# Performance work log

Hardware: AMD Instinct MI355X
Metric: run time of the kernel (lower is better)

## Reference

```python
import jax, jax.numpy as jnp
import numpy as np

B, S, D, H = 2, 2048, 1024, 16
HD = D // H
NEG_INF = jnp.finfo(jnp.float32).min


def setup_inputs() -> dict:
    key = jax.random.key(0)
    ks = jax.random.split(key, 6)
    s = 1.0 / np.sqrt(D)
    return {
        'x': jax.random.normal(ks[0], (B, S, D), dtype=jnp.float32),
        'Wq': jax.random.normal(ks[1], (D, D), dtype=jnp.float32) * s,
        'Wk': jax.random.normal(ks[2], (D, D), dtype=jnp.float32) * s,
        'Wv': jax.random.normal(ks[3], (D, D), dtype=jnp.float32) * s,
        'Wo': jax.random.normal(ks[4], (D, D), dtype=jnp.float32) * s,
        'bo': jnp.zeros((D,), dtype=jnp.float32),
    }


def reference(x, Wq, Wk, Wv, Wo, bo):
    b, s, _ = x.shape
    scale = HD ** -0.5
    # Q/K/V projections: einsum('bnd,di->bni') == x @ W
    def proj(W):
        return jnp.einsum('bnd,di->bni', x, W).reshape(b, s, H, HD).transpose(0, 2, 1, 3)
    Q, K, V = proj(Wq), proj(Wk), proj(Wv)  # [b,h,s,hd]
    scores = jnp.einsum('bhnd,bhmd->bhnm', Q, K) * scale  # [b,h,s,s]
    causal = jnp.tril(jnp.ones((s, s), dtype=bool))
    scores = jnp.where(causal[None, None], scores, NEG_INF)
    attn = jax.nn.softmax(scores, axis=-1)
    ctx = jnp.einsum('bhnm,bhmd->bhnd', attn, V)
    ctx = ctx.transpose(0, 2, 1, 3).reshape(b, s, D)
    # nn.Linear: ctx @ Wo.T + bo
    return jnp.einsum('bnd,od->bno', ctx, Wo) + bo
```

## Files before the change

### kernel.cpp

```cpp
#include <hip/hip_runtime.h>

#define B_  2
#define S_  2048
#define D_  1024
#define H_  16
#define HD_ 64
#define M_  (B_*S_)

typedef __attribute__((ext_vector_type(8))) short s16x8;
typedef __attribute__((ext_vector_type(4))) float f32x4;
typedef __attribute__((ext_vector_type(16))) float f32x16;

__device__ __forceinline__ unsigned short f2bf(float f) {
  unsigned int u = __builtin_bit_cast(unsigned int, f);
  u += 0x7fffu + ((u >> 16) & 1u);
  return (unsigned short)(u >> 16);
}

__device__ __forceinline__ void gload_lds16(const unsigned short* g, unsigned short* l) {
  __builtin_amdgcn_global_load_lds((const __attribute__((address_space(1))) void*)g,
                                   (__attribute__((address_space(3))) void*)l, 16, 0, 0);
}

__global__ void cvt_kernel(const float* __restrict__ in, unsigned short* __restrict__ out, int n4) {
  int i = blockIdx.x * blockDim.x + threadIdx.x;
  if (i >= n4) return;
  float4 v = reinterpret_cast<const float4*>(in)[i];
  ushort4 o;
  o.x = f2bf(v.x); o.y = f2bf(v.y); o.z = f2bf(v.z); o.w = f2bf(v.w);
  reinterpret_cast<ushort4*>(out)[i] = o;
}

__global__ void transpose_cvt3(const float* __restrict__ W0, const float* __restrict__ W1,
                               const float* __restrict__ W2, unsigned short* __restrict__ dstBase) {
  __shared__ float tile[32][33];
  const float* in = blockIdx.z == 0 ? W0 : (blockIdx.z == 1 ? W1 : W2);
  unsigned short* out = dstBase + (size_t)blockIdx.z * 1024 * 1024;
  const int bx = blockIdx.x, by = blockIdx.y, tx = threadIdx.x;
  const int x = bx * 32 + tx;
  for (int j = threadIdx.y; j < 32; j += 8)
    tile[j][tx] = in[(by * 32 + j) * 1024 + x];
  __syncthreads();
  const int xo = by * 32 + tx;
  for (int j = threadIdx.y; j < 32; j += 8)
    out[(bx * 32 + j) * 1024 + xo] = f2bf(tile[tx][j]);
}

#define BM 128
#define BN 128
#define BK 64

__global__ __launch_bounds__(256, 4) void gemm_bt(
    const unsigned short* __restrict__ A,
    const unsigned short* __restrict__ Bt,
    void* __restrict__ out0, void* __restrict__ out1, void* __restrict__ out2,
    const float* __restrict__ bias,
    const int mode, const float qscale)
{
  __shared__ unsigned short As[BM * BK];
  __shared__ unsigned short Bs[BN * BK];

  const int t    = threadIdx.x;
  const int lane = t & 63;
  const int wid  = t >> 6;
  const int l15  = lane & 15;
  const int g    = lane >> 4;
  const int wm   = wid >> 1;
  const int wn   = wid & 1;

  const int n0 = blockIdx.x * BN;
  const int m0 = blockIdx.y * BM;

  const int lrow = lane >> 3;
  const int lcol = ((lane & 7) ^ lrow) * 8;
  const int rsw  = l15 & 7;

  f32x4 acc[4][4];
#pragma unroll
  for (int i = 0; i < 4; ++i)
#pragma unroll
    for (int j = 0; j < 4; ++j)
      acc[i][j] = (f32x4){0.f, 0.f, 0.f, 0.f};

  for (int kt = 0; kt < 1024 / BK; ++kt) {
    const int k0 = kt * BK;
#pragma unroll
    for (int p = 0; p < 4; ++p) {
      const int c = p * 4 + wid;
      const int row = c * 8 + lrow;
      gload_lds16(&A[(size_t)(m0 + row) * 1024 + k0 + lcol], &As[c * 512]);
      gload_lds16(&Bt[(size_t)(n0 + row) * 1024 + k0 + lcol], &Bs[c * 512]);
    }
    __syncthreads();

#pragma unroll
    for (int kk = 0; kk < 2; ++kk) {
      s16x8 af[4], bf[4];
#pragma unroll
      for (int mi = 0; mi < 4; ++mi)
        af[mi] = *reinterpret_cast<const s16x8*>(
            &As[(wm * 64 + mi * 16 + l15) * BK + (((4 * kk + g) ^ rsw) * 8)]);
#pragma unroll
      for (int ni = 0; ni < 4; ++ni)
        bf[ni] = *reinterpret_cast<const s16x8*>(
            &Bs[(wn * 64 + ni * 16 + l15) * BK + (((4 * kk + g) ^ rsw) * 8)]);
#pragma unroll
      for (int mi = 0; mi < 4; ++mi)
#pragma unroll
        for (int ni = 0; ni < 4; ++ni)
          acc[mi][ni] = __builtin_amdgcn_mfma_f32_16x16x32_bf16(af[mi], bf[ni], acc[mi][ni], 0, 0, 0);
    }
    __syncthreads();
  }

  if (mode == 0) {
    const int sel = n0 >> 10;
    const int nl0 = n0 & 1023;
    if (sel < 2) {
      unsigned short* outb = (unsigned short*)(sel == 0 ? out0 : out1);
      const float sc = (sel == 0) ? qscale : 1.0f;
#pragma unroll
      for (int mi = 0; mi < 4; ++mi) {
#pragma unroll
        for (int ni = 0; ni < 4; ++ni) {
          const int n = nl0 + wn * 64 + ni * 16 + l15;
          const int h = n >> 6, hd = n & 63;
#pragma unroll
          for (int r = 0; r < 4; ++r) {
            const int m = m0 + wm * 64 + mi * 16 + 4 * g + r;
            const int b = m >> 11, s = m & 2047;
            outb[(((b * H_ + h) * S_) + s) * HD_ + hd] = f2bf(acc[mi][ni][r] * sc);
          }
        }
      }
    } else {
      unsigned short* outb = (unsigned short*)out2;
#pragma unroll
      for (int mi = 0; mi < 4; ++mi) {
#pragma unroll
        for (int ni = 0; ni < 4; ++ni) {
          const int n = nl0 + wn * 64 + ni * 16 + l15;
          const int h = n >> 6, hd = n & 63;
          const int m = m0 + wm * 64 + mi * 16 + 4 * g;
          const int b = m >> 11, s = m & 2047;
          ushort4 o;
          o.x = f2bf(acc[mi][ni][0]);
          o.y = f2bf(acc[mi][ni][1]);
          o.z = f2bf(acc[mi][ni][2]);
          o.w = f2bf(acc[mi][ni][3]);
          *reinterpret_cast<ushort4*>(&outb[(((b * H_ + h) * HD_) + hd) * S_ + s]) = o;
        }
      }
    }
  } else {
    float* outf = (float*)out0;
#pragma unroll
    for (int mi = 0; mi < 4; ++mi) {
#pragma unroll
      for (int ni = 0; ni < 4; ++ni) {
        const int n = n0 + wn * 64 + ni * 16 + l15;
        const float bv = bias[n];
#pragma unroll
        for (int r = 0; r < 4; ++r) {
          const int m = m0 + wm * 64 + mi * 16 + 4 * g + r;
          outf[m * 1024 + n] = acc[mi][ni][r] + bv;
        }
      }
    }
  }
}

__global__ __launch_bounds__(256) void attn_kernel(
    const unsigned short* __restrict__ Q,
    const unsigned short* __restrict__ K,
    const unsigned short* __restrict__ VT,
    unsigned short* __restrict__ Ctx)
{
  __shared__ unsigned short Kl[2][64 * 64];
  __shared__ unsigned short Vl[2][64 * 64];
  __shared__ unsigned short Pl[4][2][32][40];

  const int t    = threadIdx.x;
  const int lane = t & 63;
  const int w    = t >> 6;
  const int q    = lane & 31;
  const int hi   = lane >> 5;

  const int bh = blockIdx.x;
  const int qb = 15 - blockIdx.y;
  const long base  = (long)bh * S_ * HD_;
  const long vbase = (long)bh * HD_ * S_;
  const int q0w = qb * 128 + w * 32;

  const int srow = lane >> 3;
  const int scol = ((lane & 7) ^ srow) * 8;
  const int swz  = (q & 7) * 8;

  s16x8 qf[4];
#pragma unroll
  for (int s = 0; s < 4; ++s)
    qf[s] = *reinterpret_cast<const s16x8*>(&Q[base + (long)(q0w + q) * HD_ + 16 * s + 8 * hi]);

  f32x16 ctx0, ctx1;
#pragma unroll
  for (int r = 0; r < 16; ++r) { ctx0[r] = 0.f; ctx1[r] = 0.f; }
  float m_run = -1e30f, l_run = 0.f;

  const int nt = 2 * qb + 2;

#pragma unroll
  for (int p = 0; p < 2; ++p) {
    const int c = 2 * w + p;
    gload_lds16(&K[base + (long)(c * 8 + srow) * HD_ + scol], &Kl[0][c * 512]);
    gload_lds16(&VT[vbase + (long)(c * 8 + srow) * S_ + scol], &Vl[0][c * 512]);
  }
  __syncthreads();

  for (int kt = 0; kt < nt; ++kt) {
    const int cur  = kt & 1;
    const int kv64 = kt * 64;

    if (kt + 1 < nt) {
      const int nk = kv64 + 64;
#pragma unroll
      for (int p = 0; p < 2; ++p) {
        const int c = 2 * w + p;
        gload_lds16(&K[base + (long)(nk + c * 8 + srow) * HD_ + scol], &Kl[cur ^ 1][c * 512]);
        gload_lds16(&VT[vbase + (long)(c * 8 + srow) * S_ + nk + scol], &Vl[cur ^ 1][c * 512]);
      }
    }

    if (kv64 <= q0w + 31) {
      f32x16 sa0, sa1;
#pragma unroll
      for (int r = 0; r < 16; ++r) { sa0[r] = 0.f; sa1[r] = 0.f; }
      __builtin_amdgcn_s_setprio(1);
#pragma unroll
      for (int s = 0; s < 4; ++s) {
        const s16x8 kb0 = *reinterpret_cast<const s16x8*>(&Kl[cur][(q) * 64 + ((16 * s + 8 * hi) ^ swz)]);
        sa0 = __builtin_amdgcn_mfma_f32_32x32x16_bf16(kb0, qf[s], sa0, 0, 0, 0);
      }
#pragma unroll
      for (int s = 0; s < 4; ++s) {
        const s16x8 kb1 = *reinterpret_cast<const s16x8*>(&Kl[cur][(32 + q) * 64 + ((16 * s + 8 * hi) ^ swz)]);
        sa1 = __builtin_amdgcn_mfma_f32_32x32x16_bf16(kb1, qf[s], sa1, 0, 0, 0);
      }
      __builtin_amdgcn_s_setprio(0);

      if (kv64 + 64 > q0w) {
#pragma unroll
        for (int r = 0; r < 16; ++r) {
          const int kl = (r & 3) + 8 * (r >> 2) + 4 * hi;
          if (kv64 + kl > q0w + q)      sa0[r] = -1e30f;
          if (kv64 + 32 + kl > q0w + q) sa1[r] = -1e30f;
        }
      }

      float mx;
      {
        float a0 = fmaxf(fmaxf(sa0[0], sa0[1]), fmaxf(sa0[2], sa0[3]));
        float a1 = fmaxf(fmaxf(sa0[4], sa0[5]), fmaxf(sa0[6], sa0[7]));
        float a2 = fmaxf(fmaxf(sa0[8], sa0[9]), fmaxf(sa0[10], sa0[11]));
        float a3 = fmaxf(fmaxf(sa0[12], sa0[13]), fmaxf(sa0[14], sa0[15]));
        float b0 = fmaxf(fmaxf(sa1[0], sa1[1]), fmaxf(sa1[2], sa1[3]));
        float b1 = fmaxf(fmaxf(sa1[4], sa1[5]), fmaxf(sa1[6], sa1[7]));
        float b2 = fmaxf(fmaxf(sa1[8], sa1[9]), fmaxf(sa1[10], sa1[11]));
        float b3 = fmaxf(fmaxf(sa1[12], sa1[13]), fmaxf(sa1[14], sa1[15]));
        mx = fmaxf(fmaxf(fmaxf(a0, a1), fmaxf(a2, a3)), fmaxf(fmaxf(b0, b1), fmaxf(b2, b3)));
        mx = fmaxf(mx, __shfl_xor(mx, 32));
      }
      const float mn = fmaxf(m_run, mx);
      const float alpha = __builtin_amdgcn_exp2f(m_run - mn);
      m_run = mn;

      float p0[16], p1[16];
#pragma unroll
      for (int r = 0; r < 16; ++r) {
        p0[r] = __builtin_amdgcn_exp2f(sa0[r] - mn);
        p1[r] = __builtin_amdgcn_exp2f(sa1[r] - mn);
      }
      float ps;
      {
        float s0 = ((p0[0] + p0[1]) + (p0[2] + p0[3])) + ((p0[4] + p0[5]) + (p0[6] + p0[7]));
        float s1 = ((p0[8] + p0[9]) + (p0[10] + p0[11])) + ((p0[12] + p0[13]) + (p0[14] + p0[15]));
        float s2 = ((p1[0] + p1[1]) + (p1[2] + p1[3])) + ((p1[4] + p1[5]) + (p1[6] + p1[7]));
        float s3 = ((p1[8] + p1[9]) + (p1[10] + p1[11])) + ((p1[12] + p1[13]) + (p1[14] + p1[15]));
        ps = (s0 + s1) + (s2 + s3);
        ps += __shfl_xor(ps, 32);
      }
      l_run = l_run * alpha + ps;
#pragma unroll
      for (int r = 0; r < 16; ++r) { ctx0[r] *= alpha; ctx1[r] *= alpha; }

#pragma unroll
      for (int c = 0; c < 4; ++c) {
        unsigned int pk01, pk23;
        asm("v_cvt_pk_bf16_f32 %0, %1, %2" : "=v"(pk01) : "v"(p0[4 * c + 0]), "v"(p0[4 * c + 1]));
        asm("v_cvt_pk_bf16_f32 %0, %1, %2" : "=v"(pk23) : "v"(p0[4 * c + 2]), "v"(p0[4 * c + 3]));
        uint2 pr; pr.x = pk01; pr.y = pk23;
        *reinterpret_cast<uint2*>(&Pl[w][0][q][8 * c + 4 * hi]) = pr;
      }
#pragma unroll
      for (int c = 0; c < 4; ++c) {
        unsigned int pk01, pk23;
        asm("v_cvt_pk_bf16_f32 %0, %1, %2" : "=v"(pk01) : "v"(p1[4 * c + 0]), "v"(p1[4 * c + 1]));
        asm("v_cvt_pk_bf16_f32 %0, %1, %2" : "=v"(pk23) : "v"(p1[4 * c + 2]), "v"(p1[4 * c + 3]));
        uint2 pr; pr.x = pk01; pr.y = pk23;
        *reinterpret_cast<uint2*>(&Pl[w][1][q][8 * c + 4 * hi]) = pr;
      }

      __builtin_amdgcn_s_setprio(1);
#pragma unroll
      for (int kc = 0; kc < 4; ++kc) {
        const s16x8 pf = *reinterpret_cast<const s16x8*>(&Pl[w][kc >> 1][q][16 * (kc & 1) + 8 * hi]);
        const s16x8 v0 = *reinterpret_cast<const s16x8*>(&Vl[cur][(q) * 64 + ((16 * kc + 8 * hi) ^ swz)]);
        ctx0 = __builtin_amdgcn_mfma_f32_32x32x16_bf16(v0, pf, ctx0, 0, 0, 0);
        const s16x8 v1 = *reinterpret_cast<const s16x8*>(&Vl[cur][(32 + q) * 64 + ((16 * kc + 8 * hi) ^ swz)]);
        ctx1 = __builtin_amdgcn_mfma_f32_32x32x16_bf16(v1, pf, ctx1, 0, 0, 0);
      }
      __builtin_amdgcn_s_setprio(0);
    }

    __syncthreads();
  }

  const int b = bh >> 4, h = bh & 15;
  const float inv = 1.f / l_run;
  unsigned short* orow = &Ctx[((long)b * S_ + q0w + q) * D_ + h * 64];
#pragma unroll
  for (int c = 0; c < 4; ++c) {
    ushort4 o0, o1;
    o0.x = f2bf(ctx0[4 * c] * inv);     o0.y = f2bf(ctx0[4 * c + 1] * inv);
    o0.z = f2bf(ctx0[4 * c + 2] * inv); o0.w = f2bf(ctx0[4 * c + 3] * inv);
    o1.x = f2bf(ctx1[4 * c] * inv);     o1.y = f2bf(ctx1[4 * c + 1] * inv);
    o1.z = f2bf(ctx1[4 * c + 2] * inv); o1.w = f2bf(ctx1[4 * c + 3] * inv);
    *reinterpret_cast<ushort4*>(&orow[8 * c + 4 * hi])      = o0;
    *reinterpret_cast<ushort4*>(&orow[32 + 8 * c + 4 * hi]) = o1;
  }
}

extern "C" void kernel_launch(void* const* d_in, const int* in_sizes, int n_in,
                              void* d_out, int out_size, void* d_ws, size_t ws_size,
                              hipStream_t stream) {
  const float* x  = (const float*)d_in[0];
  const float* Wq = (const float*)d_in[1];
  const float* Wk = (const float*)d_in[2];
  const float* Wv = (const float*)d_in[3];
  const float* Wo = (const float*)d_in[4];
  const float* bo = (const float*)d_in[5];
  float* out = (float*)d_out;

  char* ws = (char*)d_ws;
  const size_t MB = 1024 * 1024;
  unsigned short* xb  = (unsigned short*)(ws + 0 * MB);
  unsigned short* WT  = (unsigned short*)(ws + 8 * MB);
  unsigned short* Wob = (unsigned short*)(ws + 14 * MB);
  unsigned short* Qb  = (unsigned short*)(ws + 16 * MB);
  unsigned short* Kb  = (unsigned short*)(ws + 24 * MB);
  unsigned short* VTb = (unsigned short*)(ws + 32 * MB);
  unsigned short* Cx  = (unsigned short*)(ws + 40 * MB);

  cvt_kernel<<<(M_ * D_ / 4 + 255) / 256, 256, 0, stream>>>(x, xb, M_ * D_ / 4);
  cvt_kernel<<<(D_ * D_ / 4 + 255) / 256, 256, 0, stream>>>(Wo, Wob, D_ * D_ / 4);
  transpose_cvt3<<<dim3(32, 32, 3), dim3(32, 8), 0, stream>>>(Wq, Wk, Wv, WT);

  gemm_bt<<<dim3(3 * D_ / BN, M_ / BM), 256, 0, stream>>>(
      xb, WT, (void*)Qb, (void*)Kb, (void*)VTb, nullptr, 0, 0.18033688011112042f);

  attn_kernel<<<dim3(B_ * H_, S_ / 128), 256, 0, stream>>>(Qb, Kb, VTb, Cx);

  gemm_bt<<<dim3(D_ / BN, M_ / BM), 256, 0, stream>>>(
      Cx, Wob, (void*)out, nullptr, nullptr, bo, 1, 1.0f);
}
```

Baseline: 124.2 us.

## Give each attention wave two query sub-tiles to reuse K/V fragments

The attention block drops from four waves to two. Each wave now handles 64 query rows as two 32-row sub-tiles, so K and V fragments are read from LDS once per tile and reused for both sub-tiles. The online softmax also adds a lazy rescale that only updates the running max and rescales the accumulators when the new max exceeds the old one by more than 8. This cuts LDS traffic and rescale work, but doubles register pressure per wave and halves the wave count per block, which can lower occupancy and latency hiding.

```diff
diff --git a/kernel.cpp b/kernel.cpp
--- a/kernel.cpp
+++ b/kernel.cpp
@@ -170,7 +170,7 @@
   }
 }
 
-__global__ __launch_bounds__(256) void attn_kernel(
+__global__ __launch_bounds__(128) void attn_kernel(
     const unsigned short* __restrict__ Q,
     const unsigned short* __restrict__ K,
     const unsigned short* __restrict__ VT,
@@ -178,7 +178,7 @@
 {
   __shared__ unsigned short Kl[2][64 * 64];
   __shared__ unsigned short Vl[2][64 * 64];
-  __shared__ unsigned short Pl[4][2][32][40];
+  __shared__ unsigned short Pl[2][2][32][40];
 
   const int t    = threadIdx.x;
   const int lane = t & 63;
@@ -190,27 +190,32 @@
   const int qb = 15 - blockIdx.y;
   const long base  = (long)bh * S_ * HD_;
   const long vbase = (long)bh * HD_ * S_;
-  const int q0w = qb * 128 + w * 32;
+  const int q0w = qb * 128 + w * 64;
 
   const int srow = lane >> 3;
   const int scol = ((lane & 7) ^ srow) * 8;
   const int swz  = (q & 7) * 8;
 
-  s16x8 qf[4];
-#pragma unroll
-  for (int s = 0; s < 4; ++s)
-    qf[s] = *reinterpret_cast<const s16x8*>(&Q[base + (long)(q0w + q) * HD_ + 16 * s + 8 * hi]);
-
-  f32x16 ctx0, ctx1;
-#pragma unroll
-  for (int r = 0; r < 16; ++r) { ctx0[r] = 0.f; ctx1[r] = 0.f; }
-  float m_run = -1e30f, l_run = 0.f;
+  s16x8 qf[2][4];
+#pragma unroll
+  for (int sub = 0; sub < 2; ++sub)
+#pragma unroll
+    for (int s = 0; s < 4; ++s)
+      qf[sub][s] = *reinterpret_cast<const s16x8*>(
+          &Q[base + (long)(q0w + 32 * sub + q) * HD_ + 16 * s + 8 * hi]);
+
+  f32x16 c0[2], c1[2];
+#pragma unroll
+  for (int sub = 0; sub < 2; ++sub)
+#pragma unroll
+    for (int r = 0; r < 16; ++r) { c0[sub][r] = 0.f; c1[sub][r] = 0.f; }
+  float ml[2] = {-1e30f, -1e30f}, ll[2] = {0.f, 0.f};
 
   const int nt = 2 * qb + 2;
 
 #pragma unroll
-  for (int p = 0; p < 2; ++p) {
-    const int c = 2 * w + p;
+  for (int p = 0; p < 4; ++p) {
+    const int c = 4 * w + p;
     gload_lds16(&K[base + (long)(c * 8 + srow) * HD_ + scol], &Kl[0][c * 512]);
     gload_lds16(&VT[vbase + (long)(c * 8 + srow) * S_ + scol], &Vl[0][c * 512]);
   }
@@ -223,119 +228,135 @@
     if (kt + 1 < nt) {
       const int nk = kv64 + 64;
 #pragma unroll
-      for (int p = 0; p < 2; ++p) {
-        const int c = 2 * w + p;
+      for (int p = 0; p < 4; ++p) {
+        const int c = 4 * w + p;
         gload_lds16(&K[base + (long)(nk + c * 8 + srow) * HD_ + scol], &Kl[cur ^ 1][c * 512]);
         gload_lds16(&VT[vbase + (long)(c * 8 + srow) * S_ + nk + scol], &Vl[cur ^ 1][c * 512]);
       }
     }
 
-    if (kv64 <= q0w + 31) {
-      f32x16 sa0, sa1;
-#pragma unroll
-      for (int r = 0; r < 16; ++r) { sa0[r] = 0.f; sa1[r] = 0.f; }
-      __builtin_amdgcn_s_setprio(1);
-#pragma unroll
-      for (int s = 0; s < 4; ++s) {
-        const s16x8 kb0 = *reinterpret_cast<const s16x8*>(&Kl[cur][(q) * 64 + ((16 * s + 8 * hi) ^ swz)]);
-        sa0 = __builtin_amdgcn_mfma_f32_32x32x16_bf16(kb0, qf[s], sa0, 0, 0, 0);
-      }
-#pragma unroll
-      for (int s = 0; s < 4; ++s) {
-        const s16x8 kb1 = *reinterpret_cast<const s16x8*>(&Kl[cur][(32 + q) * 64 + ((16 * s + 8 * hi) ^ swz)]);
-        sa1 = __builtin_amdgcn_mfma_f32_32x32x16_bf16(kb1, qf[s], sa1, 0, 0, 0);
-      }
-      __builtin_amdgcn_s_setprio(0);
-
-      if (kv64 + 64 > q0w) {
+    if (kv64 <= q0w + 63) {
+      s16x8 kf[8], vf[8];
+#pragma unroll
+      for (int h = 0; h < 2; ++h)
+#pragma unroll
+        for (int s = 0; s < 4; ++s) {
+          kf[h * 4 + s] = *reinterpret_cast<const s16x8*>(
+              &Kl[cur][(32 * h + q) * 64 + ((16 * s + 8 * hi) ^ swz)]);
+          vf[h * 4 + s] = *reinterpret_cast<const s16x8*>(
+              &Vl[cur][(32 * h + q) * 64 + ((16 * s + 8 * hi) ^ swz)]);
+        }
+
+#pragma unroll
+      for (int sub = 0; sub < 2; ++sub) {
+        const int q0s = q0w + 32 * sub;
+        if (kv64 > q0s + 31) continue;
+
+        f32x16 sa0, sa1;
+#pragma unroll
+        for (int r = 0; r < 16; ++r) { sa0[r] = 0.f; sa1[r] = 0.f; }
+        __builtin_amdgcn_s_setprio(1);
+#pragma unroll
+        for (int s = 0; s < 4; ++s)
+          sa0 = __builtin_amdgcn_mfma_f32_32x32x16_bf16(kf[s], qf[sub][s], sa0, 0, 0, 0);
+#pragma unroll
+        for (int s = 0; s < 4; ++s)
+          sa1 = __builtin_amdgcn_mfma_f32_32x32x16_bf16(kf[4 + s], qf[sub][s], sa1, 0, 0, 0);
+        __builtin_amdgcn_s_setprio(0);
+
+        if (kv64 + 64 > q0s) {
+#pragma unroll
+          for (int r = 0; r < 16; ++r) {
+            const int kl = (r & 3) + 8 * (r >> 2) + 4 * hi;
+            if (kv64 + kl > q0s + q)      sa0[r] = -1e30f;
+            if (kv64 + 32 + kl > q0s + q) sa1[r] = -1e30f;
+          }
+        }
+
+        float mx;
+        {
+          float a0 = fmaxf(fmaxf(sa0[0], sa0[1]), fmaxf(sa0[2], sa0[3]));
+          float a1 = fmaxf(fmaxf(sa0[4], sa0[5]), fmaxf(sa0[6], sa0[7]));
+          float a2 = fmaxf(fmaxf(sa0[8], sa0[9]), fmaxf(sa0[10], sa0[11]));
+          float a3 = fmaxf(fmaxf(sa0[12], sa0[13]), fmaxf(sa0[14], sa0[15]));
+          float b0 = fmaxf(fmaxf(sa1[0], sa1[1]), fmaxf(sa1[2], sa1[3]));
+          float b1 = fmaxf(fmaxf(sa1[4], sa1[5]), fmaxf(sa1[6], sa1[7]));
+          float b2 = fmaxf(fmaxf(sa1[8], sa1[9]), fmaxf(sa1[10], sa1[11]));
+          float b3 = fmaxf(fmaxf(sa1[12], sa1[13]), fmaxf(sa1[14], sa1[15]));
+          mx = fmaxf(fmaxf(fmaxf(a0, a1), fmaxf(a2, a3)), fmaxf(fmaxf(b0, b1), fmaxf(b2, b3)));
+          mx = fmaxf(mx, __shfl_xor(mx, 32));
+        }
+        if (mx > ml[sub] + 8.f) {
+          const float alpha = __builtin_amdgcn_exp2f(ml[sub] - mx);
+          ml[sub] = mx;
+          ll[sub] *= alpha;
+#pragma unroll
+          for (int r = 0; r < 16; ++r) { c0[sub][r] *= alpha; c1[sub][r] *= alpha; }
+        }
+
+        float p0[16], p1[16];
 #pragma unroll
         for (int r = 0; r < 16; ++r) {
-          const int kl = (r & 3) + 8 * (r >> 2) + 4 * hi;
-          if (kv64 + kl > q0w + q)      sa0[r] = -1e30f;
-          if (kv64 + 32 + kl > q0w + q) sa1[r] = -1e30f;
-        }
-      }
-
-      float mx;
-      {
-        float a0 = fmaxf(fmaxf(sa0[0], sa0[1]), fmaxf(sa0[2], sa0[3]));
-        float a1 = fmaxf(fmaxf(sa0[4], sa0[5]), fmaxf(sa0[6], sa0[7]));
-        float a2 = fmaxf(fmaxf(sa0[8], sa0[9]), fmaxf(sa0[10], sa0[11]));
-        float a3 = fmaxf(fmaxf(sa0[12], sa0[13]), fmaxf(sa0[14], sa0[15]));
-        float b0 = fmaxf(fmaxf(sa1[0], sa1[1]), fmaxf(sa1[2], sa1[3]));
-        float b1 = fmaxf(fmaxf(sa1[4], sa1[5]), fmaxf(sa1[6], sa1[7]));
-        float b2 = fmaxf(fmaxf(sa1[8], sa1[9]), fmaxf(sa1[10], sa1[11]));
-        float b3 = fmaxf(fmaxf(sa1[12], sa1[13]), fmaxf(sa1[14], sa1[15]));
-        mx = fmaxf(fmaxf(fmaxf(a0, a1), fmaxf(a2, a3)), fmaxf(fmaxf(b0, b1), fmaxf(b2, b3)));
-        mx = fmaxf(mx, __shfl_xor(mx, 32));
-      }
-      const float mn = fmaxf(m_run, mx);
-      const float alpha = __builtin_amdgcn_exp2f(m_run - mn);
-      m_run = mn;
-
-      float p0[16], p1[16];
-#pragma unroll
-      for (int r = 0; r < 16; ++r) {
-        p0[r] = __builtin_amdgcn_exp2f(sa0[r] - mn);
-        p1[r] = __builtin_amdgcn_exp2f(sa1[r] - mn);
-      }
-      float ps;
-      {
-        float s0 = ((p0[0] + p0[1]) + (p0[2] + p0[3])) + ((p0[4] + p0[5]) + (p0[6] + p0[7]));
-        float s1 = ((p0[8] + p0[9]) + (p0[10] + p0[11])) + ((p0[12] + p0[13]) + (p0[14] + p0[15]));
-        float s2 = ((p1[0] + p1[1]) + (p1[2] + p1[3])) + ((p1[4] + p1[5]) + (p1[6] + p1[7]));
-        float s3 = ((p1[8] + p1[9]) + (p1[10] + p1[11])) + ((p1[12] + p1[13]) + (p1[14] + p1[15]));
-        ps = (s0 + s1) + (s2 + s3);
-        ps += __shfl_xor(ps, 32);
-      }
-      l_run = l_run * alpha + ps;
-#pragma unroll
-      for (int r = 0; r < 16; ++r) { ctx0[r] *= alpha; ctx1[r] *= alpha; }
-
-#pragma unroll
-      for (int c = 0; c < 4; ++c) {
-        unsigned int pk01, pk23;
-        asm("v_cvt_pk_bf16_f32 %0, %1, %2" : "=v"(pk01) : "v"(p0[4 * c + 0]), "v"(p0[4 * c + 1]));
-        asm("v_cvt_pk_bf16_f32 %0, %1, %2" : "=v"(pk23) : "v"(p0[4 * c + 2]), "v"(p0[4 * c + 3]));
-        uint2 pr; pr.x = pk01; pr.y = pk23;
-        *reinterpret_cast<uint2*>(&Pl[w][0][q][8 * c + 4 * hi]) = pr;
-      }
-#pragma unroll
-      for (int c = 0; c < 4; ++c) {
-        unsigned int pk01, pk23;
-        asm("v_cvt_pk_bf16_f32 %0, %1, %2" : "=v"(pk01) : "v"(p1[4 * c + 0]), "v"(p1[4 * c + 1]));
-        asm("v_cvt_pk_bf16_f32 %0, %1, %2" : "=v"(pk23) : "v"(p1[4 * c + 2]), "v"(p1[4 * c + 3]));
-        uint2 pr; pr.x = pk01; pr.y = pk23;
-        *reinterpret_cast<uint2*>(&Pl[w][1][q][8 * c + 4 * hi]) = pr;
-      }
-
-      __builtin_amdgcn_s_setprio(1);
-#pragma unroll
-      for (int kc = 0; kc < 4; ++kc) {
-        const s16x8 pf = *reinterpret_cast<const s16x8*>(&Pl[w][kc >> 1][q][16 * (kc & 1) + 8 * hi]);
-        const s16x8 v0 = *reinterpret_cast<const s16x8*>(&Vl[cur][(q) * 64 + ((16 * kc + 8 * hi) ^ swz)]);
-        ctx0 = __builtin_amdgcn_mfma_f32_32x32x16_bf16(v0, pf, ctx0, 0, 0, 0);
-        const s16x8 v1 = *reinterpret_cast<const s16x8*>(&Vl[cur][(32 + q) * 64 + ((16 * kc + 8 * hi) ^ swz)]);
-        ctx1 = __builtin_amdgcn_mfma_f32_32x32x16_bf16(v1, pf, ctx1, 0, 0, 0);
-      }
-      __builtin_amdgcn_s_setprio(0);
+          p0[r] = __builtin_amdgcn_exp2f(sa0[r] - ml[sub]);
+          p1[r] = __builtin_amdgcn_exp2f(sa1[r] - ml[sub]);
+        }
+        float ps;
+        {
+          float s0 = ((p0[0] + p0[1]) + (p0[2] + p0[3])) + ((p0[4] + p0[5]) + (p0[6] + p0[7]));
+          float s1 = ((p0[8] + p0[9]) + (p0[10] + p0[11])) + ((p0[12] + p0[13]) + (p0[14] + p0[15]));
+          float s2 = ((p1[0] + p1[1]) + (p1[2] + p1[3])) + ((p1[4] + p1[5]) + (p1[6] + p1[7]));
+          float s3 = ((p1[8] + p1[9]) + (p1[10] + p1[11])) + ((p1[12] + p1[13]) + (p1[14] + p1[15]));
+          ps = (s0 + s1) + (s2 + s3);
+          ps += __shfl_xor(ps, 32);
+        }
+        ll[sub] += ps;
+
+#pragma unroll
+        for (int c = 0; c < 4; ++c) {
+          unsigned int pk01, pk23;
+          asm("v_cvt_pk_bf16_f32 %0, %1, %2" : "=v"(pk01) : "v"(p0[4 * c + 0]), "v"(p0[4 * c + 1]));
+          asm("v_cvt_pk_bf16_f32 %0, %1, %2" : "=v"(pk23) : "v"(p0[4 * c + 2]), "v"(p0[4 * c + 3]));
+          uint2 pr; pr.x = pk01; pr.y = pk23;
+          *reinterpret_cast<uint2*>(&Pl[w][0][q][8 * c + 4 * hi]) = pr;
+        }
+#pragma unroll
+        for (int c = 0; c < 4; ++c) {
+          unsigned int pk01, pk23;
+          asm("v_cvt_pk_bf16_f32 %0, %1, %2" : "=v"(pk01) : "v"(p1[4 * c + 0]), "v"(p1[4 * c + 1]));
+          asm("v_cvt_pk_bf16_f32 %0, %1, %2" : "=v"(pk23) : "v"(p1[4 * c + 2]), "v"(p1[4 * c + 3]));
+          uint2 pr; pr.x = pk01; pr.y = pk23;
+          *reinterpret_cast<uint2*>(&Pl[w][1][q][8 * c + 4 * hi]) = pr;
+        }
+
+        __builtin_amdgcn_s_setprio(1);
+#pragma unroll
+        for (int kc = 0; kc < 4; ++kc) {
+          const s16x8 pf = *reinterpret_cast<const s16x8*>(&Pl[w][kc >> 1][q][16 * (kc & 1) + 8 * hi]);
+          c0[sub] = __builtin_amdgcn_mfma_f32_32x32x16_bf16(vf[kc], pf, c0[sub], 0, 0, 0);
+          c1[sub] = __builtin_amdgcn_mfma_f32_32x32x16_bf16(vf[4 + kc], pf, c1[sub], 0, 0, 0);
+        }
+        __builtin_amdgcn_s_setprio(0);
+      }
     }
 
     __syncthreads();
   }
 
   const int b = bh >> 4, h = bh & 15;
-  const float inv = 1.f / l_run;
-  unsigned short* orow = &Ctx[((long)b * S_ + q0w + q) * D_ + h * 64];
-#pragma unroll
-  for (int c = 0; c < 4; ++c) {
-    ushort4 o0, o1;
-    o0.x = f2bf(ctx0[4 * c] * inv);     o0.y = f2bf(ctx0[4 * c + 1] * inv);
-    o0.z = f2bf(ctx0[4 * c + 2] * inv); o0.w = f2bf(ctx0[4 * c + 3] * inv);
-    o1.x = f2bf(ctx1[4 * c] * inv);     o1.y = f2bf(ctx1[4 * c + 1] * inv);
-    o1.z = f2bf(ctx1[4 * c + 2] * inv); o1.w = f2bf(ctx1[4 * c + 3] * inv);
-    *reinterpret_cast<ushort4*>(&orow[8 * c + 4 * hi])      = o0;
-    *reinterpret_cast<ushort4*>(&orow[32 + 8 * c + 4 * hi]) = o1;
+#pragma unroll
+  for (int sub = 0; sub < 2; ++sub) {
+    const float inv = 1.f / ll[sub];
+    unsigned short* orow = &Ctx[((long)b * S_ + q0w + 32 * sub + q) * D_ + h * 64];
+#pragma unroll
+    for (int c = 0; c < 4; ++c) {
+      ushort4 o0, o1;
+      o0.x = f2bf(c0[sub][4 * c] * inv);     o0.y = f2bf(c0[sub][4 * c + 1] * inv);
+      o0.z = f2bf(c0[sub][4 * c + 2] * inv); o0.w = f2bf(c0[sub][4 * c + 3] * inv);
+      o1.x = f2bf(c1[sub][4 * c] * inv);     o1.y = f2bf(c1[sub][4 * c + 1] * inv);
+      o1.z = f2bf(c1[sub][4 * c + 2] * inv); o1.w = f2bf(c1[sub][4 * c + 3] * inv);
+      *reinterpret_cast<ushort4*>(&orow[8 * c + 4 * hi])      = o0;
+      *reinterpret_cast<ushort4*>(&orow[32 + 8 * c + 4 * hi]) = o1;
+    }
   }
 }
 
@@ -367,7 +388,7 @@
   gemm_bt<<<dim3(3 * D_ / BN, M_ / BM), 256, 0, stream>>>(
       xb, WT, (void*)Qb, (void*)Kb, (void*)VTb, nullptr, 0, 0.18033688011112042f);
 
-  attn_kernel<<<dim3(B_ * H_, S_ / 128), 256, 0, stream>>>(Qb, Kb, VTb, Cx);
+  attn_kernel<<<dim3(B_ * H_, S_ / 128), 128, 0, stream>>>(Qb, Kb, VTb, Cx);
 
   gemm_bt<<<dim3(D_ / BN, M_ / BM), 256, 0, stream>>>(
       Cx, Wob, (void*)out, nullptr, nullptr, bo, 1, 1.0f);
```

Measured after the change: 154.7 us. +24.6%, slower.
